# Optimization experiments

Measured on AMD Instinct MI355X. Metric: run time of the kernel, lower is better.

Reference implementation:

```python
import jax, jax.numpy as jnp
import numpy as np

B, S, H = 2, 2048, 4096
NH, HD = 32, 128          # heads, head_dim = H // NH
ROPE_THETA = 10000.0
CLIP_QKV = 8.0
SCALE = HD ** -0.5


def setup_inputs() -> dict:
    key = jax.random.key(0)
    k1, k2, k3 = jax.random.split(key, 3)
    hidden_states = jax.random.normal(k1, (B, S, H), dtype=jnp.float32)
    positions = jnp.arange(S, dtype=jnp.int32)
    # 0.02 init scale keeps qkv magnitudes realistic so the +/-8 clamp rarely saturates
    w_qkv = jax.random.normal(k2, (3 * H, H), dtype=jnp.float32) * 0.02
    w_o = jax.random.normal(k3, (H, H), dtype=jnp.float32) * 0.02
    return {"hidden_states": hidden_states, "positions": positions,
            "w_qkv": w_qkv, "w_o": w_o}


def _rope(x, positions):
    # x: [B, S, NH, HD]; neox-style rotary over full head_dim
    half = HD // 2
    inv_freq = 1.0 / (ROPE_THETA ** (jnp.arange(0, half, dtype=jnp.float32) / half))
    ang = positions.astype(jnp.float32)[:, None] * inv_freq[None, :]  # [S, half]
    cos = jnp.cos(ang)[None, :, None, :]
    sin = jnp.sin(ang)[None, :, None, :]
    x1, x2 = x[..., :half], x[..., half:]
    return jnp.concatenate([x1 * cos - x2 * sin, x2 * cos + x1 * sin], axis=-1)


def reference(hidden_states, positions, w_qkv, w_o):
    # fused QKV projection (no bias) + clamp
    qkv = jnp.einsum('bsh,oh->bso', hidden_states, w_qkv)
    qkv = jnp.clip(qkv, -CLIP_QKV, CLIP_QKV)
    q, k, v = jnp.split(qkv, 3, axis=-1)            # each [B, S, H]
    q = q.reshape(B, S, NH, HD)
    k = k.reshape(B, S, NH, HD)
    v = v.reshape(B, S, NH, HD)
    q = _rope(q, positions)
    k = _rope(k, positions)
    # causal attention
    scores = jnp.einsum('bqhd,bkhd->bhqk', q, k) * SCALE
    causal = jnp.tril(jnp.ones((S, S), dtype=bool))
    scores = jnp.where(causal[None, None], scores, jnp.finfo(scores.dtype).min)
    probs = jax.nn.softmax(scores, axis=-1)
    attn = jnp.einsum('bhqk,bkhd->bqhd', probs, v).reshape(B, S, H)
    return jnp.einsum('bsh,oh->bso', attn, w_o)
```

## Files before the change

kernel.cpp:

```cpp
#include <hip/hip_runtime.h>
#include <hip/hip_bf16.h>

#define BATCH 2
#define SEQ 2048
#define HID 4096
#define NHEAD 32
#define HDIM 128
#define BH (BATCH*NHEAD)
#define MROWS (BATCH*SEQ)
#define SC2 0.1275187963f

typedef __attribute__((ext_vector_type(8))) short bf16x8;
typedef __attribute__((ext_vector_type(4))) float f32x4;

__device__ __forceinline__ float bf2f(short x){
  union { float f; unsigned u; } v; v.u = ((unsigned)(unsigned short)x) << 16; return v.f;
}
__device__ __forceinline__ short f2bf(float f){
  union { float f; unsigned u; } v; v.f = f;
  unsigned r = v.u + 0x7fffu + ((v.u >> 16) & 1u);
  return (short)(r >> 16);
}
__device__ __forceinline__ void gload_lds16(const void* g, void* l){
  __builtin_amdgcn_global_load_lds(
    (const __attribute__((address_space(1))) void*)g,
    (__attribute__((address_space(3))) void*)l, 16, 0, 0);
}

__global__ void cvt3_bf16(const float* __restrict__ a, short* __restrict__ ao, int na4,
                          const float* __restrict__ b, short* __restrict__ bo, int nb4,
                          const float* __restrict__ cc, short* __restrict__ co, int nc4){
  int i = blockIdx.x*blockDim.x + threadIdx.x;
  int stride = gridDim.x*blockDim.x;
  int tot = na4 + nb4 + nc4;
  for (; i < tot; i += stride){
    const float* src; short* dst; int k = i;
    if (k < na4){ src=a; dst=ao; }
    else if (k < na4+nb4){ k -= na4; src=b; dst=bo; }
    else { k -= na4+nb4; src=cc; dst=co; }
    float4 v = ((const float4*)src)[k];
    short4 o;
    o.x = f2bf(v.x); o.y = f2bf(v.y); o.z = f2bf(v.z); o.w = f2bf(v.w);
    ((short4*)dst)[k] = o;
  }
}

__global__ void rope_table_k(const int* __restrict__ pos, float* __restrict__ tab){
  int idx = blockIdx.x*blockDim.x + threadIdx.x;
  if (idx >= SEQ*64) return;
  int s = idx >> 6, d = idx & 63;
  float p = (float)pos[s];
  float inv = exp2f(-(float)d * (13.287712379549449f/64.0f));
  float ang = p * inv;
  tab[2*idx]   = cosf(ang);
  tab[2*idx+1] = sinf(ang);
}

template<int W>
__device__ __forceinline__ void stage_half(const short* __restrict__ gsrc, int ldg,
                                           short* lds, int tid, int h){
  #pragma unroll
  for (int li=0; li<2; ++li){
    int e16 = li*512 + tid;
    int rs = e16 >> 3, ck = e16 & 7;
    int r = ((rs/W)*2 + h)*W + (rs%W);
    gload_lds16(gsrc + (size_t)r*ldg + ((ck ^ (r&7))<<3),
                lds + r*64 + ck*8);
  }
}

__device__ __forceinline__ void read_ahalf(const short* Asb, int wr, int c, int g,
                                           int Mh, bf16x8 (&afr)[4][2]){
  #pragma unroll
  for (int mi=0; mi<4; ++mi){
    int row = wr*128 + (Mh*4+mi)*16 + c;
    const char* bp = (const char*)Asb + row*128;
    #pragma unroll
    for (int kk=0; kk<2; ++kk)
      afr[mi][kk] = *(const bf16x8*)(bp + ((kk*64 + g*16) ^ ((row&7)<<4)));
  }
}
__device__ __forceinline__ void read_bhalf(const short* Bsb, int wc, int c, int g,
                                           int Nh, bf16x8 (&bfr)[2][2]){
  #pragma unroll
  for (int ni=0; ni<2; ++ni){
    int row = wc*64 + (Nh*2+ni)*16 + c;
    const char* bp = (const char*)Bsb + row*128;
    #pragma unroll
    for (int kk=0; kk<2; ++kk)
      bfr[ni][kk] = *(const bf16x8*)(bp + ((kk*64 + g*16) ^ ((row&7)<<4)));
  }
}
template<int MH, int NHH>
__device__ __forceinline__ void mma_q(bf16x8 (&afr)[4][2], bf16x8 (&bfr)[2][2],
                                      f32x4 (&acc)[8][4]){
  #pragma unroll
  for (int kk=0; kk<2; ++kk)
    #pragma unroll
    for (int mi=0; mi<4; ++mi)
      #pragma unroll
      for (int ni=0; ni<2; ++ni)
        acc[MH*4+mi][NHH*2+ni] = __builtin_amdgcn_mfma_f32_16x16x32_bf16(
            afr[mi][kk], bfr[ni][kk], acc[MH*4+mi][NHH*2+ni], 0,0,0);
}

#define BAR()  asm volatile("s_barrier" ::: "memory")
#define LGK0() asm volatile("s_waitcnt lgkmcnt(0)" ::: "memory")
#define VMC6() asm volatile("s_waitcnt vmcnt(6)" ::: "memory")
#define VMC8() asm volatile("s_waitcnt vmcnt(8)" ::: "memory")
#define VMC0() asm volatile("s_waitcnt vmcnt(0)" ::: "memory")
#define SP1()  __builtin_amdgcn_s_setprio(1)
#define SP0()  __builtin_amdgcn_s_setprio(0)

template<int MODE>
__global__ __launch_bounds__(512, 2) void gemm8r(
    const short* __restrict__ A, const short* __restrict__ Bw,
    short* __restrict__ Qb, short* __restrict__ Kb, short* __restrict__ Vb,
    float* __restrict__ Of){
  __shared__ __align__(16) short As[2][256*64];
  __shared__ __align__(16) short Bs[2][256*64];
  const int K = HID;
  int tid = threadIdx.x, lane = tid & 63, w = tid >> 6;
  int wr = w >> 2, wc = w & 3, g = lane >> 4, c = lane & 15;
  int gx = gridDim.x;
  int nwg = gx * gridDim.y;
  int bid = blockIdx.y*gx + blockIdx.x;
  int cpx = nwg >> 3;
  int swz = (bid & 7)*cpx + (bid >> 3);
  int m0 = (swz / gx) * 256, n0 = (swz % gx) * 256;

  const short* Abase = A  + (size_t)m0*K;
  const short* Bbase = Bw + (size_t)n0*K;
  auto stageA = [&](int buf, int kt, int h){
    stage_half<64>(Abase + kt*64, K, &As[buf][0], tid, h);
  };
  auto stageB = [&](int buf, int kt, int h){
    stage_half<32>(Bbase + kt*64, K, &Bs[buf][0], tid, h);
  };

  f32x4 acc[8][4];
  f32x4 zero = {0.f,0.f,0.f,0.f};
  #pragma unroll
  for (int i=0;i<8;++i)
    #pragma unroll
    for (int j=0;j<4;++j) acc[i][j] = zero;
  bf16x8 afr[4][2], bfr0[2][2], bfr1[2][2];

  stageB(0,0,0); stageB(0,0,1); stageA(0,0,0); stageA(0,0,1);
  stageB(1,1,0); stageB(1,1,1); stageA(1,1,0); stageA(1,1,1);
  VMC8();
  BAR();

  const int NITER = K/128;
  for (int i = 0; i < NITER-1; ++i){
    int t2 = 2*i+2, t3 = 2*i+3;
    read_ahalf(&As[0][0], wr,c,g, 0, afr);
    read_bhalf(&Bs[0][0], wc,c,g, 0, bfr0);
    BAR(); LGK0(); SP1(); mma_q<0,0>(afr,bfr0,acc); SP0(); BAR();
    read_bhalf(&Bs[0][0], wc,c,g, 1, bfr1);
    stageB(0, t2, 0);
    BAR(); LGK0(); SP1(); mma_q<0,1>(afr,bfr1,acc); SP0(); BAR();
    read_ahalf(&As[0][0], wr,c,g, 1, afr);
    stageB(0, t2, 1); stageA(0, t2, 0);
    BAR(); LGK0(); SP1(); mma_q<1,1>(afr,bfr1,acc); SP0(); BAR();
    BAR(); LGK0(); SP1(); mma_q<1,0>(afr,bfr0,acc); SP0(); VMC6(); BAR();
    read_ahalf(&As[1][0], wr,c,g, 0, afr);
    read_bhalf(&Bs[1][0], wc,c,g, 0, bfr0);
    stageA(0, t2, 1);
    BAR(); LGK0(); SP1(); mma_q<0,0>(afr,bfr0,acc); SP0(); BAR();
    read_bhalf(&Bs[1][0], wc,c,g, 1, bfr1);
    stageB(1, t3, 0);
    BAR(); LGK0(); SP1(); mma_q<0,1>(afr,bfr1,acc); SP0(); BAR();
    read_ahalf(&As[1][0], wr,c,g, 1, afr);
    stageB(1, t3, 1); stageA(1, t3, 0);
    BAR(); LGK0(); SP1(); mma_q<1,1>(afr,bfr1,acc); SP0(); BAR();
    stageA(1, t3, 1);
    BAR(); LGK0(); SP1(); mma_q<1,0>(afr,bfr0,acc); SP0(); VMC8(); BAR();
  }
  {
    read_ahalf(&As[0][0], wr,c,g, 0, afr);
    read_bhalf(&Bs[0][0], wc,c,g, 0, bfr0);
    BAR(); LGK0(); SP1(); mma_q<0,0>(afr,bfr0,acc); SP0(); BAR();
    read_bhalf(&Bs[0][0], wc,c,g, 1, bfr1);
    BAR(); LGK0(); SP1(); mma_q<0,1>(afr,bfr1,acc); SP0(); BAR();
    read_ahalf(&As[0][0], wr,c,g, 1, afr);
    BAR(); LGK0(); SP1(); mma_q<1,1>(afr,bfr1,acc); SP0(); BAR();
    BAR(); LGK0(); SP1(); mma_q<1,0>(afr,bfr0,acc); SP0(); VMC0(); BAR();
    read_ahalf(&As[1][0], wr,c,g, 0, afr);
    read_bhalf(&Bs[1][0], wc,c,g, 0, bfr0);
    BAR(); LGK0(); SP1(); mma_q<0,0>(afr,bfr0,acc); SP0(); BAR();
    read_bhalf(&Bs[1][0], wc,c,g, 1, bfr1);
    BAR(); LGK0(); SP1(); mma_q<0,1>(afr,bfr1,acc); SP0(); BAR();
    read_ahalf(&As[1][0], wr,c,g, 1, afr);
    BAR(); LGK0(); SP1(); mma_q<1,1>(afr,bfr1,acc); SP0(); BAR();
    BAR(); LGK0(); SP1(); mma_q<1,0>(afr,bfr0,acc); SP0(); BAR();
  }

  #pragma unroll
  for (int fa=0; fa<8; ++fa){
    #pragma unroll
    for (int fb=0; fb<4; ++fb){
      f32x4 v = acc[fa][fb];
      #pragma unroll
      for (int rr=0; rr<4; ++rr){
        int row = m0 + wr*128 + fa*16 + g*4 + rr;
        int col = n0 + wc*64  + fb*16 + c;
        float x = v[rr];
        if (MODE == 0){
          x = fminf(fmaxf(x, -8.0f), 8.0f);
          int sel = col >> 12, wi = col & 4095;
          int head = wi >> 7, d = wi & 127;
          int b = row >> 11, s = row & 2047;
          size_t off = ((size_t)(b*NHEAD + head)*SEQ + s)*HDIM + d;
          short* dst = (sel == 0) ? Qb : (sel == 1) ? Kb : Vb;
          dst[off] = f2bf(x);
        } else {
          Of[(size_t)row*HID + col] = x;
        }
      }
    }
  }
}

__global__ void rope_apply_k(short* __restrict__ Qb, short* __restrict__ Kb,
                             const float* __restrict__ tab){
  int idx = blockIdx.x*blockDim.x + threadIdx.x;
  if (idx >= BH*SEQ*8) return;
  int t = idx & 7;
  int s = (idx >> 3) & (SEQ-1);
  int bh = idx >> 14;
  size_t base = ((size_t)bh*SEQ + s)*HDIM + t*8;
  const float* tb = tab + 2*(s*64 + t*8);
  bf16x8 q1 = *(bf16x8*)(Qb+base), q2 = *(bf16x8*)(Qb+base+64);
  bf16x8 k1 = *(bf16x8*)(Kb+base), k2 = *(bf16x8*)(Kb+base+64);
  bf16x8 o1, o2, p1, p2;
  #pragma unroll
  for (int u=0;u<8;++u){
    float cs = tb[2*u], sn = tb[2*u+1];
    float a = bf2f(q1[u]), b = bf2f(q2[u]);
    o1[u] = f2bf(a*cs - b*sn); o2[u] = f2bf(b*cs + a*sn);
    a = bf2f(k1[u]); b = bf2f(k2[u]);
    p1[u] = f2bf(a*cs - b*sn); p2[u] = f2bf(b*cs + a*sn);
  }
  *(bf16x8*)(Qb+base)    = o1; *(bf16x8*)(Qb+base+64) = o2;
  *(bf16x8*)(Kb+base)    = p1; *(bf16x8*)(Kb+base+64) = p2;
}

__global__ void transpose_v_k(const short* __restrict__ V, short* __restrict__ Vt){
  __shared__ short t[32][33];
  int bh = blockIdx.z;
  int s0 = blockIdx.x*32, d0 = blockIdx.y*32;
  int tx = threadIdx.x & 31, ty = threadIdx.x >> 5;
  const short* src = V + ((size_t)bh*SEQ + s0)*HDIM + d0;
  #pragma unroll
  for (int i=ty;i<32;i+=8) t[i][tx] = src[(size_t)i*HDIM + tx];
  __syncthreads();
  short* dst = Vt + ((size_t)bh*HDIM + d0)*SEQ + s0;
  #pragma unroll
  for (int i=ty;i<32;i+=8) dst[(size_t)i*SEQ + tx] = t[tx][i];
}

__global__ __launch_bounds__(512, 4) void flash_attn2_k(
    const short* __restrict__ Qb, const short* __restrict__ Kb,
    const short* __restrict__ Vt, short* __restrict__ attn){
  __shared__ short Ks[2][64*128];
  __shared__ short Vs[2][128*64];
  __shared__ short Ps[8][16][64];
  int tid = threadIdx.x, lane = tid & 63, w = tid >> 6;
  int g = lane >> 4, c = lane & 15;
  int flat = blockIdx.x;
  int xcd = flat & 7, idx = flat >> 3;
  int bh = xcd + 8*(idx >> 4);
  int jq = idx & 15;
  int qw = jq*128 + w*16;
  bf16x8 qf[4];
  #pragma unroll
  for (int ks=0;ks<4;++ks)
    qf[ks] = *(const bf16x8*)(Qb + ((size_t)bh*SEQ + qw + c)*HDIM + ks*32 + g*8);
  f32x4 o[8];
  f32x4 zero = {0.f,0.f,0.f,0.f};
  #pragma unroll
  for (int i=0;i<8;++i) o[i] = zero;
  float m_r[4] = {-1e30f,-1e30f,-1e30f,-1e30f};
  float l_r[4] = {0.f,0.f,0.f,0.f};

  auto stage = [&](int j, int b){
    int kv0 = j*64;
    #pragma unroll
    for (int i=0;i<2;++i){
      int e = i*512 + tid;
      int kr = e >> 4, kc = e & 15;
      gload_lds16(Kb + ((size_t)bh*SEQ + kv0 + kr)*HDIM + (size_t)((kc ^ (kr&7))*8),
                  &Ks[b][kr*128 + kc*8]);
      int vr = e >> 3, vc = e & 7;
      gload_lds16(Vt + ((size_t)bh*HDIM + vr)*SEQ + kv0 + (size_t)((vc ^ (vr&7))*8),
                  &Vs[b][vr*64 + vc*8]);
    }
  };

  const int jmaxb = 2*jq + 1;
  const int jmaxw = (qw + 15) >> 6;

  stage(0, 0);
  __syncthreads();
  int buf = 0;
  for (int j=0; j<=jmaxb; ++j){
    if (j < jmaxb) stage(j+1, buf^1);
    if (j <= jmaxw){
      int kv0 = j*64;
      f32x4 sf[4];
      #pragma unroll
      for (int fj=0;fj<4;++fj) sf[fj] = zero;
      __builtin_amdgcn_s_setprio(1);
      #pragma unroll
      for (int ks=0;ks<4;++ks){
        #pragma unroll
        for (int fj=0;fj<4;++fj){
          int kvrow = fj*16 + c;
          bf16x8 kb = *(const bf16x8*)&Ks[buf][kvrow*128 + (((ks*4+g) ^ (c&7))*8)];
          sf[fj] = __builtin_amdgcn_mfma_f32_16x16x32_bf16(qf[ks], kb, sf[fj], 0,0,0);
        }
      }
      __builtin_amdgcn_s_setprio(0);
      bool diag = (j == jmaxw);
      float rmax[4];
      #pragma unroll
      for (int rr=0;rr<4;++rr){
        #pragma unroll
        for (int fj=0;fj<4;++fj){
          float v = sf[fj][rr] * SC2;
          if (diag && (kv0 + fj*16 + c) > (qw + g*4 + rr)) v = -1e30f;
          sf[fj][rr] = v;
        }
        float t = fmaxf(fmaxf(sf[0][rr], sf[1][rr]), fmaxf(sf[2][rr], sf[3][rr]));
        t = fmaxf(t, __shfl_xor(t, 1));
        t = fmaxf(t, __shfl_xor(t, 2));
        t = fmaxf(t, __shfl_xor(t, 4));
        t = fmaxf(t, __shfl_xor(t, 8));
        rmax[rr] = t;
      }
      bool need = (rmax[0] > m_r[0] + 8.0f) | (rmax[1] > m_r[1] + 8.0f) |
                  (rmax[2] > m_r[2] + 8.0f) | (rmax[3] > m_r[3] + 8.0f);
      if (__any(need)){
        float alpha[4];
        #pragma unroll
        for (int rr=0;rr<4;++rr){
          float mnew = fmaxf(m_r[rr], rmax[rr]);
          alpha[rr] = exp2f(m_r[rr] - mnew);
          m_r[rr] = mnew;
          l_r[rr] *= alpha[rr];
        }
        #pragma unroll
        for (int ni=0;ni<8;++ni){
          f32x4 t = o[ni];
          t[0]*=alpha[0]; t[1]*=alpha[1]; t[2]*=alpha[2]; t[3]*=alpha[3];
          o[ni] = t;
        }
      }
      #pragma unroll
      for (int rr=0;rr<4;++rr){
        float ps = 0.f;
        #pragma unroll
        for (int fj=0;fj<4;++fj){
          float p = exp2f(sf[fj][rr] - m_r[rr]);
          sf[fj][rr] = p;
          ps += p;
        }
        ps += __shfl_xor(ps, 1);
        ps += __shfl_xor(ps, 2);
        ps += __shfl_xor(ps, 4);
        ps += __shfl_xor(ps, 8);
        l_r[rr] += ps;
      }
      #pragma unroll
      for (int fj=0;fj<4;++fj)
        #pragma unroll
        for (int rr=0;rr<4;++rr){
          int row = g*4 + rr;
          Ps[w][row][(fj*16+c) ^ ((row&7)<<3)] = f2bf(sf[fj][rr]);
        }
      __builtin_amdgcn_s_setprio(1);
      #pragma unroll
      for (int ks=0;ks<2;++ks){
        bf16x8 pa = *(const bf16x8*)&Ps[w][c][(ks*32 + g*8) ^ ((c&7)<<3)];
        #pragma unroll
        for (int ni=0;ni<8;++ni){
          int d = ni*16 + c;
          bf16x8 vb = *(const bf16x8*)&Vs[buf][d*64 + (((ks*4+g) ^ (c&7))*8)];
          o[ni] = __builtin_amdgcn_mfma_f32_16x16x32_bf16(pa, vb, o[ni], 0,0,0);
        }
      }
      __builtin_amdgcn_s_setprio(0);
    }
    __syncthreads();
    buf ^= 1;
  }
  int b = bh >> 5, h = bh & 31;
  #pragma unroll
  for (int rr=0;rr<4;++rr){
    float inv = 1.0f / l_r[rr];
    int s = qw + g*4 + rr;
    #pragma unroll
    for (int ni=0;ni<8;++ni){
      int d = ni*16 + c;
      attn[((size_t)(b*SEQ + s))*HID + h*HDIM + d] = f2bf(o[ni][rr] * inv);
    }
  }
}

extern "C" void kernel_launch(void* const* d_in, const int* in_sizes, int n_in,
                              void* d_out, int out_size, void* d_ws, size_t ws_size,
                              hipStream_t stream){
  const float* hs   = (const float*)d_in[0];
  const int*   pos  = (const int*)d_in[1];
  const float* wqkv = (const float*)d_in[2];
  const float* wo   = (const float*)d_in[3];
  float* out = (float*)d_out;
  char* ws = (char*)d_ws;
  size_t off = 0;
  auto alloc = [&](size_t bytes){ void* p = ws + off; off += (bytes + 255) & ~(size_t)255; return p; };
  short* hsb   = (short*)alloc((size_t)MROWS*HID*2);
  short* wqkvb = (short*)alloc((size_t)3*HID*HID*2);
  short* wob   = (short*)alloc((size_t)HID*HID*2);
  short* Qb    = (short*)alloc((size_t)BH*SEQ*HDIM*2);
  short* Kb    = (short*)alloc((size_t)BH*SEQ*HDIM*2);
  short* Vb    = (short*)alloc((size_t)BH*SEQ*HDIM*2);
  short* Vt    = (short*)alloc((size_t)BH*SEQ*HDIM*2);
  short* attn  = (short*)alloc((size_t)MROWS*HID*2);
  float* tab   = (float*)alloc((size_t)SEQ*64*2*4);
  (void)ws_size; (void)in_sizes; (void)n_in; (void)out_size;

  cvt3_bf16<<<2048,256,0,stream>>>(hs, hsb, MROWS*HID/4,
                                   wqkv, wqkvb, 3*HID*HID/4,
                                   wo, wob, HID*HID/4);
  rope_table_k<<<(SEQ*64+255)/256,256,0,stream>>>(pos, tab);
  gemm8r<0><<<dim3(48,16),512,0,stream>>>(hsb, wqkvb, Qb, Kb, Vb, nullptr);
  rope_apply_k<<<(BH*SEQ*8+255)/256,256,0,stream>>>(Qb, Kb, tab);
  transpose_v_k<<<dim3(SEQ/32, HDIM/32, BH),256,0,stream>>>(Vb, Vt);
  flash_attn2_k<<<dim3(BH*16),512,0,stream>>>(Qb, Kb, Vt, attn);
  gemm8r<1><<<dim3(16,16),512,0,stream>>>(attn, wob, nullptr, nullptr, nullptr, out);
}
```

Before: 830.6 us.

## Prefetch LDS fragments one phase ahead in GEMM and reverse attention block order

Restructures the GEMM main loop into a software-pipelined schedule. Each phase now issues LDS fragment reads for the next MFMA group before the current one runs, using double A-fragment registers, and drops the explicit lgkmcnt(0) waits. The peeled tail is folded into the loop with a predicate. Separately, flash attention now launches heavy causal query tiles first to improve load balance. The risks are higher register pressure and relying on compiler-inserted waits for LDS reads.

```diff
diff --git a/kernel.cpp b/kernel.cpp
--- a/kernel.cpp
+++ b/kernel.cpp
@@ -105,7 +105,6 @@
 }
 
 #define BAR()  asm volatile("s_barrier" ::: "memory")
-#define LGK0() asm volatile("s_waitcnt lgkmcnt(0)" ::: "memory")
 #define VMC6() asm volatile("s_waitcnt vmcnt(6)" ::: "memory")
 #define VMC8() asm volatile("s_waitcnt vmcnt(8)" ::: "memory")
 #define VMC0() asm volatile("s_waitcnt vmcnt(0)" ::: "memory")
@@ -113,7 +112,7 @@
 #define SP0()  __builtin_amdgcn_s_setprio(0)
 
 template<int MODE>
-__global__ __launch_bounds__(512, 2) void gemm8r(
+__global__ __launch_bounds__(512, 2) void gemm8p2(
     const short* __restrict__ A, const short* __restrict__ Bw,
     short* __restrict__ Qb, short* __restrict__ Kb, short* __restrict__ Vb,
     float* __restrict__ Of){
@@ -144,56 +143,47 @@
   for (int i=0;i<8;++i)
     #pragma unroll
     for (int j=0;j<4;++j) acc[i][j] = zero;
-  bf16x8 afr[4][2], bfr0[2][2], bfr1[2][2];
+  bf16x8 afrX[4][2], afrY[4][2], bfr0[2][2], bfr1[2][2];
 
   stageB(0,0,0); stageB(0,0,1); stageA(0,0,0); stageA(0,0,1);
   stageB(1,1,0); stageB(1,1,1); stageA(1,1,0); stageA(1,1,1);
   VMC8();
   BAR();
+  read_ahalf(&As[0][0], wr,c,g, 0, afrX);
+  read_bhalf(&Bs[0][0], wc,c,g, 0, bfr0);
 
   const int NITER = K/128;
-  for (int i = 0; i < NITER-1; ++i){
+  for (int i = 0; i < NITER; ++i){
     int t2 = 2*i+2, t3 = 2*i+3;
-    read_ahalf(&As[0][0], wr,c,g, 0, afr);
-    read_bhalf(&Bs[0][0], wc,c,g, 0, bfr0);
-    BAR(); LGK0(); SP1(); mma_q<0,0>(afr,bfr0,acc); SP0(); BAR();
+    bool st = (i < NITER-1);
     read_bhalf(&Bs[0][0], wc,c,g, 1, bfr1);
-    stageB(0, t2, 0);
-    BAR(); LGK0(); SP1(); mma_q<0,1>(afr,bfr1,acc); SP0(); BAR();
-    read_ahalf(&As[0][0], wr,c,g, 1, afr);
-    stageB(0, t2, 1); stageA(0, t2, 0);
-    BAR(); LGK0(); SP1(); mma_q<1,1>(afr,bfr1,acc); SP0(); BAR();
-    BAR(); LGK0(); SP1(); mma_q<1,0>(afr,bfr0,acc); SP0(); VMC6(); BAR();
-    read_ahalf(&As[1][0], wr,c,g, 0, afr);
+    BAR(); SP1(); mma_q<0,0>(afrX,bfr0,acc); SP0(); BAR();
+    read_ahalf(&As[0][0], wr,c,g, 1, afrY);
+    if (st){ stageA(0,t2,0); stageB(0,t2,0); }
+    BAR(); SP1(); mma_q<0,1>(afrX,bfr1,acc); SP0(); BAR();
+    if (st) stageB(0,t2,1);
+    BAR(); SP1(); mma_q<1,1>(afrY,bfr1,acc); SP0();
+    if (st) { VMC6(); } else { VMC0(); }
+    BAR();
+    read_ahalf(&As[1][0], wr,c,g, 0, afrX);
+    if (st) stageA(0,t2,1);
+    BAR(); SP1(); mma_q<1,0>(afrY,bfr0,acc); SP0();
     read_bhalf(&Bs[1][0], wc,c,g, 0, bfr0);
-    stageA(0, t2, 1);
-    BAR(); LGK0(); SP1(); mma_q<0,0>(afr,bfr0,acc); SP0(); BAR();
+    BAR();
     read_bhalf(&Bs[1][0], wc,c,g, 1, bfr1);
-    stageB(1, t3, 0);
-    BAR(); LGK0(); SP1(); mma_q<0,1>(afr,bfr1,acc); SP0(); BAR();
-    read_ahalf(&As[1][0], wr,c,g, 1, afr);
-    stageB(1, t3, 1); stageA(1, t3, 0);
-    BAR(); LGK0(); SP1(); mma_q<1,1>(afr,bfr1,acc); SP0(); BAR();
-    stageA(1, t3, 1);
-    BAR(); LGK0(); SP1(); mma_q<1,0>(afr,bfr0,acc); SP0(); VMC8(); BAR();
-  }
-  {
-    read_ahalf(&As[0][0], wr,c,g, 0, afr);
-    read_bhalf(&Bs[0][0], wc,c,g, 0, bfr0);
-    BAR(); LGK0(); SP1(); mma_q<0,0>(afr,bfr0,acc); SP0(); BAR();
-    read_bhalf(&Bs[0][0], wc,c,g, 1, bfr1);
-    BAR(); LGK0(); SP1(); mma_q<0,1>(afr,bfr1,acc); SP0(); BAR();
-    read_ahalf(&As[0][0], wr,c,g, 1, afr);
-    BAR(); LGK0(); SP1(); mma_q<1,1>(afr,bfr1,acc); SP0(); BAR();
-    BAR(); LGK0(); SP1(); mma_q<1,0>(afr,bfr0,acc); SP0(); VMC0(); BAR();
-    read_ahalf(&As[1][0], wr,c,g, 0, afr);
-    read_bhalf(&Bs[1][0], wc,c,g, 0, bfr0);
-    BAR(); LGK0(); SP1(); mma_q<0,0>(afr,bfr0,acc); SP0(); BAR();
-    read_bhalf(&Bs[1][0], wc,c,g, 1, bfr1);
-    BAR(); LGK0(); SP1(); mma_q<0,1>(afr,bfr1,acc); SP0(); BAR();
-    read_ahalf(&As[1][0], wr,c,g, 1, afr);
-    BAR(); LGK0(); SP1(); mma_q<1,1>(afr,bfr1,acc); SP0(); BAR();
-    BAR(); LGK0(); SP1(); mma_q<1,0>(afr,bfr0,acc); SP0(); BAR();
+    BAR(); SP1(); mma_q<0,0>(afrX,bfr0,acc); SP0(); BAR();
+    read_ahalf(&As[1][0], wr,c,g, 1, afrY);
+    if (st){ stageA(1,t3,0); stageB(1,t3,0); }
+    BAR(); SP1(); mma_q<0,1>(afrX,bfr1,acc); SP0(); BAR();
+    if (st) stageB(1,t3,1);
+    BAR(); SP1(); mma_q<1,1>(afrY,bfr1,acc); SP0();
+    if (st) { VMC6(); } else { VMC0(); }
+    BAR();
+    if (st) read_ahalf(&As[0][0], wr,c,g, 0, afrX);
+    if (st) stageA(1,t3,1);
+    BAR(); SP1(); mma_q<1,0>(afrY,bfr0,acc); SP0();
+    if (st) read_bhalf(&Bs[0][0], wc,c,g, 0, bfr0);
+    BAR();
   }
 
   #pragma unroll
@@ -271,7 +261,7 @@
   int flat = blockIdx.x;
   int xcd = flat & 7, idx = flat >> 3;
   int bh = xcd + 8*(idx >> 4);
-  int jq = idx & 15;
+  int jq = 15 - (idx & 15);
   int qw = jq*128 + w*16;
   bf16x8 qf[4];
   #pragma unroll
@@ -434,9 +424,9 @@
                                    wqkv, wqkvb, 3*HID*HID/4,
                                    wo, wob, HID*HID/4);
   rope_table_k<<<(SEQ*64+255)/256,256,0,stream>>>(pos, tab);
-  gemm8r<0><<<dim3(48,16),512,0,stream>>>(hsb, wqkvb, Qb, Kb, Vb, nullptr);
+  gemm8p2<0><<<dim3(48,16),512,0,stream>>>(hsb, wqkvb, Qb, Kb, Vb, nullptr);
   rope_apply_k<<<(BH*SEQ*8+255)/256,256,0,stream>>>(Qb, Kb, tab);
   transpose_v_k<<<dim3(SEQ/32, HDIM/32, BH),256,0,stream>>>(Vb, Vt);
   flash_attn2_k<<<dim3(BH*16),512,0,stream>>>(Qb, Kb, Vt, attn);
-  gemm8r<1><<<dim3(16,16),512,0,stream>>>(attn, wob, nullptr, nullptr, nullptr, out);
-}
+  gemm8p2<1><<<dim3(16,16),512,0,stream>>>(attn, wob, nullptr, nullptr, nullptr, out);
+}
```

Measured after the change: 1.239 ms. 49.2% more time.

## Shrink attention blocks to 64 queries and 4 waves with reversed scheduling

Applied to the files above, without the earlier changes.

The flash attention kernel moves from 128-query, 8-wave blocks to 64-query, 4-wave blocks on a 2D grid, with query blocks issued in reverse order so the longest causal rows start first. The lazy rescale threshold and the exp2 scale folding are replaced by an unconditional rescale using __expf with the plain scale. The XOR swizzle on the P scratch buffer is replaced by a padded row stride. Each K/V tile is now shared by half as many waves, so staging traffic per unit of work doubles, and the unconditional rescale adds work on every iteration.

```diff
diff --git a/kernel.cpp b/kernel.cpp
--- a/kernel.cpp
+++ b/kernel.cpp
@@ -8,7 +8,7 @@
 #define HDIM 128
 #define BH (BATCH*NHEAD)
 #define MROWS (BATCH*SEQ)
-#define SC2 0.1275187963f
+#define ATT_SCALE 0.08838834764831845f
 
 typedef __attribute__((ext_vector_type(8))) short bf16x8;
 typedef __attribute__((ext_vector_type(4))) float f32x4;
@@ -260,19 +260,20 @@
   for (int i=ty;i<32;i+=8) dst[(size_t)i*SEQ + tx] = t[tx][i];
 }
 
-__global__ __launch_bounds__(512, 4) void flash_attn2_k(
+__global__ __launch_bounds__(256) void flash_attn_k(
     const short* __restrict__ Qb, const short* __restrict__ Kb,
     const short* __restrict__ Vt, short* __restrict__ attn){
   __shared__ short Ks[2][64*128];
   __shared__ short Vs[2][128*64];
-  __shared__ short Ps[8][16][64];
+  __shared__ short Ps[4][16][72];
   int tid = threadIdx.x, lane = tid & 63, w = tid >> 6;
   int g = lane >> 4, c = lane & 15;
-  int flat = blockIdx.x;
+  int flat = blockIdx.y*gridDim.x + blockIdx.x;
   int xcd = flat & 7, idx = flat >> 3;
-  int bh = xcd + 8*(idx >> 4);
-  int jq = idx & 15;
-  int qw = jq*128 + w*16;
+  int bh = xcd + 8*(idx >> 5);
+  int qblk = 31 - (idx & 31);
+  int q0 = qblk * 64;
+  int qw = q0 + w*16;
   bf16x8 qf[4];
   #pragma unroll
   for (int ks=0;ks<4;++ks)
@@ -287,8 +288,8 @@
   auto stage = [&](int j, int b){
     int kv0 = j*64;
     #pragma unroll
-    for (int i=0;i<2;++i){
-      int e = i*512 + tid;
+    for (int i=0;i<4;++i){
+      int e = i*256 + tid;
       int kr = e >> 4, kc = e & 15;
       gload_lds16(Kb + ((size_t)bh*SEQ + kv0 + kr)*HDIM + (size_t)((kc ^ (kr&7))*8),
                   &Ks[b][kr*128 + kc*8]);
@@ -298,100 +299,86 @@
     }
   };
 
-  const int jmaxb = 2*jq + 1;
-  const int jmaxw = (qw + 15) >> 6;
-
   stage(0, 0);
   __syncthreads();
   int buf = 0;
-  for (int j=0; j<=jmaxb; ++j){
-    if (j < jmaxb) stage(j+1, buf^1);
-    if (j <= jmaxw){
-      int kv0 = j*64;
-      f32x4 sf[4];
-      #pragma unroll
-      for (int fj=0;fj<4;++fj) sf[fj] = zero;
-      __builtin_amdgcn_s_setprio(1);
-      #pragma unroll
-      for (int ks=0;ks<4;++ks){
-        #pragma unroll
-        for (int fj=0;fj<4;++fj){
-          int kvrow = fj*16 + c;
-          bf16x8 kb = *(const bf16x8*)&Ks[buf][kvrow*128 + (((ks*4+g) ^ (c&7))*8)];
-          sf[fj] = __builtin_amdgcn_mfma_f32_16x16x32_bf16(qf[ks], kb, sf[fj], 0,0,0);
-        }
+  for (int j=0;j<=qblk;++j){
+    if (j < qblk) stage(j+1, buf^1);
+
+    int kv0 = j*64;
+    f32x4 sf[4];
+    #pragma unroll
+    for (int fj=0;fj<4;++fj) sf[fj] = zero;
+    __builtin_amdgcn_s_setprio(1);
+    #pragma unroll
+    for (int ks=0;ks<4;++ks){
+      #pragma unroll
+      for (int fj=0;fj<4;++fj){
+        int kvrow = fj*16 + c;
+        bf16x8 kb = *(const bf16x8*)&Ks[buf][kvrow*128 + (((ks*4+g) ^ (c&7))*8)];
+        sf[fj] = __builtin_amdgcn_mfma_f32_16x16x32_bf16(qf[ks], kb, sf[fj], 0,0,0);
       }
-      __builtin_amdgcn_s_setprio(0);
-      bool diag = (j == jmaxw);
-      float rmax[4];
-      #pragma unroll
-      for (int rr=0;rr<4;++rr){
-        #pragma unroll
-        for (int fj=0;fj<4;++fj){
-          float v = sf[fj][rr] * SC2;
-          if (diag && (kv0 + fj*16 + c) > (qw + g*4 + rr)) v = -1e30f;
-          sf[fj][rr] = v;
-        }
-        float t = fmaxf(fmaxf(sf[0][rr], sf[1][rr]), fmaxf(sf[2][rr], sf[3][rr]));
-        t = fmaxf(t, __shfl_xor(t, 1));
-        t = fmaxf(t, __shfl_xor(t, 2));
-        t = fmaxf(t, __shfl_xor(t, 4));
-        t = fmaxf(t, __shfl_xor(t, 8));
-        rmax[rr] = t;
+    }
+    __builtin_amdgcn_s_setprio(0);
+    bool diag = (j == qblk);
+    float rmax[4];
+    #pragma unroll
+    for (int rr=0;rr<4;++rr){
+      #pragma unroll
+      for (int fj=0;fj<4;++fj){
+        float v = sf[fj][rr] * ATT_SCALE;
+        if (diag && (kv0 + fj*16 + c) > (qw + g*4 + rr)) v = -1e30f;
+        sf[fj][rr] = v;
       }
-      bool need = (rmax[0] > m_r[0] + 8.0f) | (rmax[1] > m_r[1] + 8.0f) |
-                  (rmax[2] > m_r[2] + 8.0f) | (rmax[3] > m_r[3] + 8.0f);
-      if (__any(need)){
-        float alpha[4];
-        #pragma unroll
-        for (int rr=0;rr<4;++rr){
-          float mnew = fmaxf(m_r[rr], rmax[rr]);
-          alpha[rr] = exp2f(m_r[rr] - mnew);
-          m_r[rr] = mnew;
-          l_r[rr] *= alpha[rr];
-        }
-        #pragma unroll
-        for (int ni=0;ni<8;++ni){
-          f32x4 t = o[ni];
-          t[0]*=alpha[0]; t[1]*=alpha[1]; t[2]*=alpha[2]; t[3]*=alpha[3];
-          o[ni] = t;
-        }
+      float t = fmaxf(fmaxf(sf[0][rr], sf[1][rr]), fmaxf(sf[2][rr], sf[3][rr]));
+      t = fmaxf(t, __shfl_xor(t, 1));
+      t = fmaxf(t, __shfl_xor(t, 2));
+      t = fmaxf(t, __shfl_xor(t, 4));
+      t = fmaxf(t, __shfl_xor(t, 8));
+      rmax[rr] = t;
+    }
+    float alpha[4];
+    #pragma unroll
+    for (int rr=0;rr<4;++rr){
+      float mnew = fmaxf(m_r[rr], rmax[rr]);
+      alpha[rr] = __expf(m_r[rr] - mnew);
+      m_r[rr] = mnew;
+      float ps = 0.f;
+      #pragma unroll
+      for (int fj=0;fj<4;++fj){
+        float p = __expf(sf[fj][rr] - mnew);
+        sf[fj][rr] = p;
+        ps += p;
       }
-      #pragma unroll
-      for (int rr=0;rr<4;++rr){
-        float ps = 0.f;
-        #pragma unroll
-        for (int fj=0;fj<4;++fj){
-          float p = exp2f(sf[fj][rr] - m_r[rr]);
-          sf[fj][rr] = p;
-          ps += p;
-        }
-        ps += __shfl_xor(ps, 1);
-        ps += __shfl_xor(ps, 2);
-        ps += __shfl_xor(ps, 4);
-        ps += __shfl_xor(ps, 8);
-        l_r[rr] += ps;
+      ps += __shfl_xor(ps, 1);
+      ps += __shfl_xor(ps, 2);
+      ps += __shfl_xor(ps, 4);
+      ps += __shfl_xor(ps, 8);
+      l_r[rr] = l_r[rr]*alpha[rr] + ps;
+    }
+    #pragma unroll
+    for (int ni=0;ni<8;++ni){
+      f32x4 t = o[ni];
+      t[0]*=alpha[0]; t[1]*=alpha[1]; t[2]*=alpha[2]; t[3]*=alpha[3];
+      o[ni] = t;
+    }
+    #pragma unroll
+    for (int fj=0;fj<4;++fj)
+      #pragma unroll
+      for (int rr=0;rr<4;++rr)
+        Ps[w][g*4+rr][fj*16+c] = f2bf(sf[fj][rr]);
+    __builtin_amdgcn_s_setprio(1);
+    #pragma unroll
+    for (int ks=0;ks<2;++ks){
+      bf16x8 pa = *(const bf16x8*)&Ps[w][c][ks*32 + g*8];
+      #pragma unroll
+      for (int ni=0;ni<8;++ni){
+        int d = ni*16 + c;
+        bf16x8 vb = *(const bf16x8*)&Vs[buf][d*64 + (((ks*4+g) ^ (c&7))*8)];
+        o[ni] = __builtin_amdgcn_mfma_f32_16x16x32_bf16(pa, vb, o[ni], 0,0,0);
       }
-      #pragma unroll
-      for (int fj=0;fj<4;++fj)
-        #pragma unroll
-        for (int rr=0;rr<4;++rr){
-          int row = g*4 + rr;
-          Ps[w][row][(fj*16+c) ^ ((row&7)<<3)] = f2bf(sf[fj][rr]);
-        }
-      __builtin_amdgcn_s_setprio(1);
-      #pragma unroll
-      for (int ks=0;ks<2;++ks){
-        bf16x8 pa = *(const bf16x8*)&Ps[w][c][(ks*32 + g*8) ^ ((c&7)<<3)];
-        #pragma unroll
-        for (int ni=0;ni<8;++ni){
-          int d = ni*16 + c;
-          bf16x8 vb = *(const bf16x8*)&Vs[buf][d*64 + (((ks*4+g) ^ (c&7))*8)];
-          o[ni] = __builtin_amdgcn_mfma_f32_16x16x32_bf16(pa, vb, o[ni], 0,0,0);
-        }
-      }
-      __builtin_amdgcn_s_setprio(0);
-    }
+    }
+    __builtin_amdgcn_s_setprio(0);
     __syncthreads();
     buf ^= 1;
   }
@@ -437,6 +424,6 @@
   gemm8r<0><<<dim3(48,16),512,0,stream>>>(hsb, wqkvb, Qb, Kb, Vb, nullptr);
   rope_apply_k<<<(BH*SEQ*8+255)/256,256,0,stream>>>(Qb, Kb, tab);
   transpose_v_k<<<dim3(SEQ/32, HDIM/32, BH),256,0,stream>>>(Vb, Vt);
-  flash_attn2_k<<<dim3(BH*16),512,0,stream>>>(Qb, Kb, Vt, attn);
+  flash_attn_k<<<dim3(SEQ/64, BH),256,0,stream>>>(Qb, Kb, Vt, attn);
   gemm8r<1><<<dim3(16,16),512,0,stream>>>(attn, wob, nullptr, nullptr, nullptr, out);
 }
```

After: 819.0 us. Within noise of the previous version (-1.4%).
